# Kernel tuning notes

Hardware: AMD Instinct MI355X
Metric: run time of the kernel (lower is better)

The kernel has to match this reference:

```python
import jax, jax.numpy as jnp
import numpy as np
from jax.scipy.special import logsumexp

EPSILON = 0.1
MAX_ITER = 100
LOG_CLAMP = 1e-30  # matches torch _log_safe clamp(min=1e-30)


def setup_inputs() -> dict:
    key = jax.random.key(0)
    k_c, k_a, k_b = jax.random.split(key, 3)
    B, M, N = 16, 2048, 2048
    C = jax.random.uniform(k_c, (B, M, N), dtype=jnp.float32)  # nonnegative cost matrix
    a = jax.random.uniform(k_a, (B, M), dtype=jnp.float32) + 0.1
    a = a / a.sum(axis=1, keepdims=True)  # source marginal, sums to 1 per batch
    b = jax.random.uniform(k_b, (B, N), dtype=jnp.float32) + 0.1
    b = b / b.sum(axis=1, keepdims=True)  # target marginal
    return {"C": C, "a": a, "b": b}


def reference(C, a, b):
    """Log-domain balanced Sinkhorn (SinkhornDistance.forward, epsilon_scaling=False).

    Returns (distance: (B,), P: (B, M, N)).
    Runs a fixed MAX_ITER iterations (the torch early-break with tol=1e-6 is a
    host-sync convergence shortcut to the same fixed point).
    """
    log_a = jnp.log(jnp.clip(a, LOG_CLAMP))  # (B, M)
    log_b = jnp.log(jnp.clip(b, LOG_CLAMP))  # (B, N)
    log_K = -C / EPSILON  # (B, M, N)
    B, M, N = C.shape
    u0 = jnp.zeros((B, M), dtype=C.dtype)
    v0 = jnp.zeros((B, N), dtype=C.dtype)

    def step(carry, _):
        u, v = carry
        u = log_a - logsumexp(log_K + v[:, None, :], axis=2)  # (B, M)
        v = log_b - logsumexp(log_K + u[:, :, None], axis=1)  # (B, N)
        return (u, v), None

    (u, v), _ = jax.lax.scan(step, (u0, v0), None, length=MAX_ITER)
    log_P = u[:, :, None] + log_K + v[:, None, :]  # (B, M, N)
    P = jnp.exp(log_P)
    distance = jnp.sum(P * C, axis=(1, 2))  # (B,)
    return distance, P
```

## Files before the change

kernel.cpp:

```cpp
#include <hip/hip_runtime.h>
#include <hip/hip_fp16.h>

namespace {

constexpr int NB = 16;
constexpr int MM = 2048;
constexpr int NN = 2048;
constexpr float NEG_INV_EPS = -10.0f;
constexpr int ITERS = 100;


__global__ void __launch_bounds__(256) build_k(const float* __restrict__ C,
                                               __half* __restrict__ K) {
  const size_t stride = (size_t)gridDim.x * blockDim.x * 8;
  const size_t total = (size_t)NB * MM * NN;
  for (size_t i = ((size_t)blockIdx.x * blockDim.x + threadIdx.x) * 8;
       i < total; i += stride) {
    float4 c0 = *reinterpret_cast<const float4*>(C + i);
    float4 c1 = *reinterpret_cast<const float4*>(C + i + 4);
    __half2 h[4];
    h[0] = __floats2half2_rn(__expf(NEG_INV_EPS * c0.x), __expf(NEG_INV_EPS * c0.y));
    h[1] = __floats2half2_rn(__expf(NEG_INV_EPS * c0.z), __expf(NEG_INV_EPS * c0.w));
    h[2] = __floats2half2_rn(__expf(NEG_INV_EPS * c1.x), __expf(NEG_INV_EPS * c1.y));
    h[3] = __floats2half2_rn(__expf(NEG_INV_EPS * c1.z), __expf(NEG_INV_EPS * c1.w));
    *reinterpret_cast<uint4*>(K + i) = *reinterpret_cast<uint4*>(h);
  }
}


__global__ void __launch_bounds__(512, 4) sink_iter_h(
    const __half* __restrict__ Kp,
    const float* __restrict__ a, const float* __restrict__ bm,
    const float* __restrict__ s_cur, float* __restrict__ s_acc,
    float* __restrict__ s_zero, float* __restrict__ z_out) {
  __shared__ __align__(16) __half ksh[2][8][NN];
  __shared__ __align__(16) float wsh[NN];
  __shared__ float zsh[2][8];
  const int b = blockIdx.x >> 5;
  const int chunk = blockIdx.x & 31;
  const int tid = threadIdx.x;
  const int bbase = b * NN;

  {
    const float4 b4 = *reinterpret_cast<const float4*>(bm + bbase + tid * 4);
    const float4 s4 = *reinterpret_cast<const float4*>(s_cur + bbase + tid * 4);
    float4 w4;
    w4.x = b4.x * __builtin_amdgcn_rcpf(s4.x);
    w4.y = b4.y * __builtin_amdgcn_rcpf(s4.y);
    w4.z = b4.z * __builtin_amdgcn_rcpf(s4.z);
    w4.w = b4.w * __builtin_amdgcn_rcpf(s4.w);
    *reinterpret_cast<float4*>(&wsh[tid * 4]) = w4;
  }
  if (tid < 64) s_zero[bbase + chunk * 64 + tid] = 0.0f;
  __syncthreads();

  const int wave = tid >> 6;
  const int lane = tid & 63;

  float wreg[32];
#pragma unroll
  for (int k = 0; k < 4; ++k) {
    const float4* w4 = reinterpret_cast<const float4*>(&wsh[k * 512 + lane * 8]);
    const float4 wa = w4[0], wb = w4[1];
    wreg[k * 8 + 0] = wa.x; wreg[k * 8 + 1] = wa.y;
    wreg[k * 8 + 2] = wa.z; wreg[k * 8 + 3] = wa.w;
    wreg[k * 8 + 4] = wb.x; wreg[k * 8 + 5] = wb.y;
    wreg[k * 8 + 6] = wb.z; wreg[k * 8 + 7] = wb.w;
  }

  const int r0 = chunk * 64;
  const int mycol = tid * 4;
  const size_t abase = (size_t)b * MM;
  float colacc[4] = {0.f, 0.f, 0.f, 0.f};
  uint4 kr[4];

  {
    const int row = r0 + wave;
    const size_t kb = (abase + row) * NN;
    const float av = a[abase + row];
#pragma unroll
    for (int k = 0; k < 4; ++k)
      kr[k] = *reinterpret_cast<const uint4*>(Kp + kb + k * 512 + lane * 8);
    float acc = 0.f;
#pragma unroll
    for (int k = 0; k < 4; ++k) {
      *reinterpret_cast<uint4*>(&ksh[0][wave][k * 512 + lane * 8]) = kr[k];
      const __half2* h = reinterpret_cast<const __half2*>(&kr[k]);
      const float2 f0 = __half22float2(h[0]);
      const float2 f1 = __half22float2(h[1]);
      const float2 f2 = __half22float2(h[2]);
      const float2 f3 = __half22float2(h[3]);
      acc += f0.x * wreg[k * 8 + 0] + f0.y * wreg[k * 8 + 1] +
             f1.x * wreg[k * 8 + 2] + f1.y * wreg[k * 8 + 3] +
             f2.x * wreg[k * 8 + 4] + f2.y * wreg[k * 8 + 5] +
             f3.x * wreg[k * 8 + 6] + f3.y * wreg[k * 8 + 7];
    }
#pragma unroll
    for (int off = 32; off; off >>= 1) acc += __shfl_xor(acc, off, 64);
    const float zv = av * __builtin_amdgcn_rcpf(acc);
    if (lane == 0) {
      zsh[0][wave] = zv;
      z_out[abase + row] = zv;
    }
  }
  __syncthreads();

  for (int sc = 0; sc < 8; ++sc) {
    const int cb = sc & 1, nb = cb ^ 1;
    float av = 0.f;
    if (sc < 7) {
      const int row = r0 + (sc + 1) * 8 + wave;
      const size_t kb = (abase + row) * NN;
      av = a[abase + row];
#pragma unroll
      for (int k = 0; k < 4; ++k)
        kr[k] = *reinterpret_cast<const uint4*>(Kp + kb + k * 512 + lane * 8);
    }
#pragma unroll
    for (int r = 0; r < 8; ++r) {
      const float zi = zsh[cb][r];
      uint2 rv = *reinterpret_cast<const uint2*>(&ksh[cb][r][mycol]);
      const __half2* h = reinterpret_cast<const __half2*>(&rv);
      const float2 f01 = __half22float2(h[0]);
      const float2 f23 = __half22float2(h[1]);
      colacc[0] += f01.x * zi;
      colacc[1] += f01.y * zi;
      colacc[2] += f23.x * zi;
      colacc[3] += f23.y * zi;
    }
    if (sc < 7) {
      const int row = r0 + (sc + 1) * 8 + wave;
      float acc = 0.f;
#pragma unroll
      for (int k = 0; k < 4; ++k) {
        *reinterpret_cast<uint4*>(&ksh[nb][wave][k * 512 + lane * 8]) = kr[k];
        const __half2* h = reinterpret_cast<const __half2*>(&kr[k]);
        const float2 f0 = __half22float2(h[0]);
        const float2 f1 = __half22float2(h[1]);
        const float2 f2 = __half22float2(h[2]);
        const float2 f3 = __half22float2(h[3]);
        acc += f0.x * wreg[k * 8 + 0] + f0.y * wreg[k * 8 + 1] +
               f1.x * wreg[k * 8 + 2] + f1.y * wreg[k * 8 + 3] +
               f2.x * wreg[k * 8 + 4] + f2.y * wreg[k * 8 + 5] +
               f3.x * wreg[k * 8 + 6] + f3.y * wreg[k * 8 + 7];
      }
#pragma unroll
      for (int off = 32; off; off >>= 1) acc += __shfl_xor(acc, off, 64);
      const float zv = av * __builtin_amdgcn_rcpf(acc);
      if (lane == 0) {
        zsh[nb][wave] = zv;
        z_out[abase + row] = zv;
      }
    }
    __syncthreads();
  }

  float* s = s_acc + bbase + mycol;
#pragma unroll
  for (int m = 0; m < 4; ++m) atomicAdd(&s[m], colacc[m]);
}


struct KFromC {
  const float* p;
  __device__ __forceinline__ void load8h(size_t i, float* o, uint4* raw) const {
    float4 c0 = *reinterpret_cast<const float4*>(p + i);
    float4 c1 = *reinterpret_cast<const float4*>(p + i + 4);
    o[0] = __expf(NEG_INV_EPS * c0.x); o[1] = __expf(NEG_INV_EPS * c0.y);
    o[2] = __expf(NEG_INV_EPS * c0.z); o[3] = __expf(NEG_INV_EPS * c0.w);
    o[4] = __expf(NEG_INV_EPS * c1.x); o[5] = __expf(NEG_INV_EPS * c1.y);
    o[6] = __expf(NEG_INV_EPS * c1.z); o[7] = __expf(NEG_INV_EPS * c1.w);
    __half2 h[4];
    h[0] = __floats2half2_rn(o[0], o[1]);
    h[1] = __floats2half2_rn(o[2], o[3]);
    h[2] = __floats2half2_rn(o[4], o[5]);
    h[3] = __floats2half2_rn(o[6], o[7]);
    *raw = *reinterpret_cast<uint4*>(h);
  }
};

template <class KS>
__global__ void __launch_bounds__(512, 4) sink_iter(KS ks,
    const float* __restrict__ a, const float* __restrict__ bm,
    const float* __restrict__ s_cur, float* __restrict__ s_acc,
    float* __restrict__ s_zero, float* __restrict__ z_out) {
  __shared__ __align__(16) __half ksh[16][NN];
  __shared__ __align__(16) float wsh[NN];
  __shared__ float zsh[16];
  const int b = blockIdx.x >> 5;
  const int chunk = blockIdx.x & 31;
  const int tid = threadIdx.x;
  const int bbase = b * NN;

  {
    const float4 b4 = *reinterpret_cast<const float4*>(bm + bbase + tid * 4);
    const float4 s4 = *reinterpret_cast<const float4*>(s_cur + bbase + tid * 4);
    float4 w4;
    w4.x = b4.x * __builtin_amdgcn_rcpf(s4.x);
    w4.y = b4.y * __builtin_amdgcn_rcpf(s4.y);
    w4.z = b4.z * __builtin_amdgcn_rcpf(s4.z);
    w4.w = b4.w * __builtin_amdgcn_rcpf(s4.w);
    *reinterpret_cast<float4*>(&wsh[tid * 4]) = w4;
  }
  if (tid < 64) s_zero[bbase + chunk * 64 + tid] = 0.0f;
  __syncthreads();

  const int wave = tid >> 6;
  const int lane = tid & 63;

  float wreg[32];
#pragma unroll
  for (int k = 0; k < 4; ++k) {
    const float4* w4 = reinterpret_cast<const float4*>(&wsh[k * 512 + lane * 8]);
    const float4 wa = w4[0], wb = w4[1];
    wreg[k * 8 + 0] = wa.x; wreg[k * 8 + 1] = wa.y;
    wreg[k * 8 + 2] = wa.z; wreg[k * 8 + 3] = wa.w;
    wreg[k * 8 + 4] = wb.x; wreg[k * 8 + 5] = wb.y;
    wreg[k * 8 + 6] = wb.z; wreg[k * 8 + 7] = wb.w;
  }

  const int r0 = chunk * 64;
  const int mycol = tid * 4;
  float colacc[4] = {0.f, 0.f, 0.f, 0.f};

  for (int sc = 0; sc < 4; ++sc) {
    const int rowbase = r0 + sc * 16;
#pragma unroll
    for (int rr = 0; rr < 2; ++rr) {
      const int lrow = wave * 2 + rr;
      const int row = rowbase + lrow;
      const size_t kb = ((size_t)(b * MM + row)) * NN;
      float acc = 0.f;
#pragma unroll
      for (int k = 0; k < 4; ++k) {
        float kv[8];
        uint4 raw;
        ks.load8h(kb + k * 512 + lane * 8, kv, &raw);
        *reinterpret_cast<uint4*>(&ksh[lrow][k * 512 + lane * 8]) = raw;
#pragma unroll
        for (int m = 0; m < 8; ++m) acc += kv[m] * wreg[k * 8 + m];
      }
#pragma unroll
      for (int off = 32; off; off >>= 1) acc += __shfl_xor(acc, off, 64);
      if (lane == 0) {
        const float zv = a[b * MM + row] * __builtin_amdgcn_rcpf(acc);
        zsh[lrow] = zv;
        z_out[b * MM + row] = zv;
      }
    }
    __syncthreads();
#pragma unroll 4
    for (int r = 0; r < 16; ++r) {
      const float zi = zsh[r];
      uint2 rv = *reinterpret_cast<const uint2*>(&ksh[r][mycol]);
      const __half2* h = reinterpret_cast<const __half2*>(&rv);
      const float2 f01 = __half22float2(h[0]);
      const float2 f23 = __half22float2(h[1]);
      colacc[0] += f01.x * zi;
      colacc[1] += f01.y * zi;
      colacc[2] += f23.x * zi;
      colacc[3] += f23.y * zi;
    }
    __syncthreads();
  }

  float* s = s_acc + bbase + mycol;
#pragma unroll
  for (int m = 0; m < 4; ++m) atomicAdd(&s[m], colacc[m]);
}


__global__ void __launch_bounds__(256) final_pass(const float* __restrict__ C,
    const float* __restrict__ z, const float* __restrict__ bm,
    const float* __restrict__ s_fin, float* __restrict__ out) {
  __shared__ __align__(16) float wsh[NN];
  __shared__ float zsh[16];
  __shared__ float red[256];
  const int b = blockIdx.x >> 7;
  const int rc = blockIdx.x & 127;
  const int tid = threadIdx.x;
  const int bbase = b * NN;

  for (int j = tid; j < NN; j += 256)
    wsh[j] = bm[bbase + j] * __builtin_amdgcn_rcpf(s_fin[bbase + j]);
  if (tid < 16) zsh[tid] = z[b * MM + rc * 16 + tid];
  __syncthreads();

  float* __restrict__ P = out + NB;
  const int col = tid * 8;
  const float4* w4 = reinterpret_cast<const float4*>(&wsh[col]);
  const float4 wa = w4[0], wb = w4[1];

  float accd = 0.0f;
#pragma unroll 4
  for (int rr = 0; rr < 16; ++rr) {
    const int row = rc * 16 + rr;
    const float zi = zsh[rr];
    const size_t base = ((size_t)(b * MM + row)) * NN + col;
    float4 c0 = *reinterpret_cast<const float4*>(C + base);
    float4 c1 = *reinterpret_cast<const float4*>(C + base + 4);
    float4 p0, p1;
    p0.x = zi * __expf(NEG_INV_EPS * c0.x) * wa.x;
    p0.y = zi * __expf(NEG_INV_EPS * c0.y) * wa.y;
    p0.z = zi * __expf(NEG_INV_EPS * c0.z) * wa.z;
    p0.w = zi * __expf(NEG_INV_EPS * c0.w) * wa.w;
    p1.x = zi * __expf(NEG_INV_EPS * c1.x) * wb.x;
    p1.y = zi * __expf(NEG_INV_EPS * c1.y) * wb.y;
    p1.z = zi * __expf(NEG_INV_EPS * c1.z) * wb.z;
    p1.w = zi * __expf(NEG_INV_EPS * c1.w) * wb.w;
    *reinterpret_cast<float4*>(P + base) = p0;
    *reinterpret_cast<float4*>(P + base + 4) = p1;
    accd += p0.x * c0.x + p0.y * c0.y + p0.z * c0.z + p0.w * c0.w +
            p1.x * c1.x + p1.y * c1.y + p1.z * c1.z + p1.w * c1.w;
  }

  red[tid] = accd;
  __syncthreads();
  if (tid < 128) red[tid] += red[tid + 128];
  __syncthreads();
  if (tid < 64) {
    float v = red[tid] + red[tid + 64];
#pragma unroll
    for (int off = 32; off; off >>= 1) v += __shfl_xor(v, off, 64);
    if (tid == 0) atomicAdd(&out[b], v);
  }
}

}

extern "C" void kernel_launch(void* const* d_in, const int* in_sizes, int n_in,
                              void* d_out, int out_size, void* d_ws, size_t ws_size,
                              hipStream_t stream) {
  const float* C  = (const float*)d_in[0];
  const float* a  = (const float*)d_in[1];
  const float* bm = (const float*)d_in[2];
  float* out = (float*)d_out;
  char* ws = (char*)d_ws;

  const size_t VEC = (size_t)NB * MM * sizeof(float);
  float* z = (float*)(ws);
  float* s[3] = {(float*)(ws + VEC), (float*)(ws + 2 * VEC), (float*)(ws + 3 * VEC)};
  __half* K = (__half*)(ws + 4 * VEC);
  const size_t needK = 4 * VEC + (size_t)NB * MM * NN * sizeof(__half);
  const bool useHalf = (ws_size >= needK);

  hipMemsetAsync(out, 0, NB * sizeof(float), stream);
  hipMemcpyAsync(s[0], bm, (size_t)NB * NN * sizeof(float),
                 hipMemcpyDeviceToDevice, stream);
  hipMemsetAsync(s[1], 0, (size_t)NB * NN * sizeof(float), stream);

  if (useHalf) {
    build_k<<<8192, 256, 0, stream>>>(C, K);
    for (int t = 0; t < ITERS; ++t) {
      sink_iter_h<<<NB * 32, 512, 0, stream>>>(
          K, a, bm, s[t % 3], s[(t + 1) % 3], s[(t + 2) % 3], z);
    }
  } else {
    KFromC ks{C};
    for (int t = 0; t < ITERS; ++t) {
      sink_iter<KFromC><<<NB * 32, 512, 0, stream>>>(
          ks, a, bm, s[t % 3], s[(t + 1) % 3], s[(t + 2) % 3], z);
    }
  }

  final_pass<<<NB * 128, 256, 0, stream>>>(C, z, bm, s[ITERS % 3], out);
}
```

Baseline: 3.594 ms.

## Fuse all Sinkhorn iterations into one cooperative persistent kernel with grid sync

Replaces the 100 separate per-iteration launches with a single cooperative kernel that loops over iterations and uses grid.sync between phases. The column-sum atomics are replaced by per-chunk partial buffers reduced deterministically after a grid barrier, with the scaled weight vector written once for the next iteration. This removes launch overhead and atomic contention but adds two grid-wide barriers per iteration, and it requires all 512 blocks to be co-resident.

```diff
diff --git a/kernel.cpp b/kernel.cpp
--- a/kernel.cpp
+++ b/kernel.cpp
@@ -1,5 +1,8 @@
 #include <hip/hip_runtime.h>
 #include <hip/hip_fp16.h>
+#include <hip/hip_cooperative_groups.h>
+
+namespace cg = cooperative_groups;
 
 namespace {
 
@@ -28,6 +31,155 @@
 }
 
 
+__global__ void __launch_bounds__(512, 4) sink_coop(
+    const __half* __restrict__ Kp,
+    const float* __restrict__ a, const float* __restrict__ bm,
+    float* __restrict__ z_out, float* __restrict__ wbuf,
+    float* __restrict__ partial) {
+  cg::grid_group grid = cg::this_grid();
+  __shared__ __align__(16) __half ksh[2][8][NN];
+  __shared__ __align__(16) float wsh[NN];
+  __shared__ float zsh[2][8];
+  const int b = blockIdx.x >> 5;
+  const int chunk = blockIdx.x & 31;
+  const int tid = threadIdx.x;
+  const int bbase = b * NN;
+  const int wave = tid >> 6;
+  const int lane = tid & 63;
+  const int r0 = chunk * 64;
+  const int mycol = tid * 4;
+  const size_t abase = (size_t)b * MM;
+
+  for (int t = 0; t < ITERS; ++t) {
+    if (t == 0) {
+      *reinterpret_cast<float4*>(&wsh[tid * 4]) = make_float4(1.f, 1.f, 1.f, 1.f);
+    } else {
+      *reinterpret_cast<float4*>(&wsh[tid * 4]) =
+          *reinterpret_cast<const float4*>(wbuf + bbase + tid * 4);
+    }
+    __syncthreads();
+
+    float wreg[32];
+#pragma unroll
+    for (int k = 0; k < 4; ++k) {
+      const float4* w4 = reinterpret_cast<const float4*>(&wsh[k * 512 + lane * 8]);
+      const float4 wa = w4[0], wb = w4[1];
+      wreg[k * 8 + 0] = wa.x; wreg[k * 8 + 1] = wa.y;
+      wreg[k * 8 + 2] = wa.z; wreg[k * 8 + 3] = wa.w;
+      wreg[k * 8 + 4] = wb.x; wreg[k * 8 + 5] = wb.y;
+      wreg[k * 8 + 6] = wb.z; wreg[k * 8 + 7] = wb.w;
+    }
+
+    const bool lastit = (t == ITERS - 1);
+    float colacc[4] = {0.f, 0.f, 0.f, 0.f};
+    uint4 kr[4];
+
+    {
+      const int row = r0 + wave;
+      const size_t kb = (abase + row) * NN;
+      const float av = a[abase + row];
+#pragma unroll
+      for (int k = 0; k < 4; ++k)
+        kr[k] = *reinterpret_cast<const uint4*>(Kp + kb + k * 512 + lane * 8);
+      float acc = 0.f;
+#pragma unroll
+      for (int k = 0; k < 4; ++k) {
+        *reinterpret_cast<uint4*>(&ksh[0][wave][k * 512 + lane * 8]) = kr[k];
+        const __half2* h = reinterpret_cast<const __half2*>(&kr[k]);
+        const float2 f0 = __half22float2(h[0]);
+        const float2 f1 = __half22float2(h[1]);
+        const float2 f2 = __half22float2(h[2]);
+        const float2 f3 = __half22float2(h[3]);
+        acc += f0.x * wreg[k * 8 + 0] + f0.y * wreg[k * 8 + 1] +
+               f1.x * wreg[k * 8 + 2] + f1.y * wreg[k * 8 + 3] +
+               f2.x * wreg[k * 8 + 4] + f2.y * wreg[k * 8 + 5] +
+               f3.x * wreg[k * 8 + 6] + f3.y * wreg[k * 8 + 7];
+      }
+#pragma unroll
+      for (int off = 32; off; off >>= 1) acc += __shfl_xor(acc, off, 64);
+      const float zv = av * __builtin_amdgcn_rcpf(acc);
+      if (lane == 0) {
+        zsh[0][wave] = zv;
+        if (lastit) z_out[abase + row] = zv;
+      }
+    }
+    __syncthreads();
+
+    for (int sc = 0; sc < 8; ++sc) {
+      const int cb = sc & 1, nb2 = cb ^ 1;
+      float av = 0.f;
+      if (sc < 7) {
+        const int row = r0 + (sc + 1) * 8 + wave;
+        const size_t kb = (abase + row) * NN;
+        av = a[abase + row];
+#pragma unroll
+        for (int k = 0; k < 4; ++k)
+          kr[k] = *reinterpret_cast<const uint4*>(Kp + kb + k * 512 + lane * 8);
+      }
+#pragma unroll
+      for (int r = 0; r < 8; ++r) {
+        const float zi = zsh[cb][r];
+        uint2 rv = *reinterpret_cast<const uint2*>(&ksh[cb][r][mycol]);
+        const __half2* h = reinterpret_cast<const __half2*>(&rv);
+        const float2 f01 = __half22float2(h[0]);
+        const float2 f23 = __half22float2(h[1]);
+        colacc[0] += f01.x * zi;
+        colacc[1] += f01.y * zi;
+        colacc[2] += f23.x * zi;
+        colacc[3] += f23.y * zi;
+      }
+      if (sc < 7) {
+        const int row = r0 + (sc + 1) * 8 + wave;
+        float acc = 0.f;
+#pragma unroll
+        for (int k = 0; k < 4; ++k) {
+          *reinterpret_cast<uint4*>(&ksh[nb2][wave][k * 512 + lane * 8]) = kr[k];
+          const __half2* h = reinterpret_cast<const __half2*>(&kr[k]);
+          const float2 f0 = __half22float2(h[0]);
+          const float2 f1 = __half22float2(h[1]);
+          const float2 f2 = __half22float2(h[2]);
+          const float2 f3 = __half22float2(h[3]);
+          acc += f0.x * wreg[k * 8 + 0] + f0.y * wreg[k * 8 + 1] +
+                 f1.x * wreg[k * 8 + 2] + f1.y * wreg[k * 8 + 3] +
+                 f2.x * wreg[k * 8 + 4] + f2.y * wreg[k * 8 + 5] +
+                 f3.x * wreg[k * 8 + 6] + f3.y * wreg[k * 8 + 7];
+        }
+#pragma unroll
+        for (int off = 32; off; off >>= 1) acc += __shfl_xor(acc, off, 64);
+        const float zv = av * __builtin_amdgcn_rcpf(acc);
+        if (lane == 0) {
+          zsh[nb2][wave] = zv;
+          if (lastit) z_out[abase + row] = zv;
+        }
+      }
+      __syncthreads();
+    }
+
+    *reinterpret_cast<float4*>(partial + ((size_t)(b * 32 + chunk)) * NN + mycol) =
+        make_float4(colacc[0], colacc[1], colacc[2], colacc[3]);
+    __threadfence();
+    grid.sync();
+
+    if (tid < 64) {
+      const int col = chunk * 64 + tid;
+      const float* pp = partial + (size_t)b * 32 * NN + col;
+      float s0 = 0.f, s1 = 0.f, s2 = 0.f, s3 = 0.f;
+#pragma unroll
+      for (int c = 0; c < 32; c += 4) {
+        s0 += pp[(size_t)(c + 0) * NN];
+        s1 += pp[(size_t)(c + 1) * NN];
+        s2 += pp[(size_t)(c + 2) * NN];
+        s3 += pp[(size_t)(c + 3) * NN];
+      }
+      const float sv = (s0 + s1) + (s2 + s3);
+      wbuf[bbase + col] = bm[bbase + col] * __builtin_amdgcn_rcpf(sv);
+    }
+    __threadfence();
+    grid.sync();
+  }
+}
+
+
 __global__ void __launch_bounds__(512, 4) sink_iter_h(
     const __half* __restrict__ Kp,
     const float* __restrict__ a, const float* __restrict__ bm,
@@ -106,7 +258,7 @@
   __syncthreads();
 
   for (int sc = 0; sc < 8; ++sc) {
-    const int cb = sc & 1, nb = cb ^ 1;
+    const int cb = sc & 1, nb2 = cb ^ 1;
     float av = 0.f;
     if (sc < 7) {
       const int row = r0 + (sc + 1) * 8 + wave;
@@ -133,7 +285,7 @@
       float acc = 0.f;
 #pragma unroll
       for (int k = 0; k < 4; ++k) {
-        *reinterpret_cast<uint4*>(&ksh[nb][wave][k * 512 + lane * 8]) = kr[k];
+        *reinterpret_cast<uint4*>(&ksh[nb2][wave][k * 512 + lane * 8]) = kr[k];
         const __half2* h = reinterpret_cast<const __half2*>(&kr[k]);
         const float2 f0 = __half22float2(h[0]);
         const float2 f1 = __half22float2(h[1]);
@@ -148,7 +300,7 @@
       for (int off = 32; off; off >>= 1) acc += __shfl_xor(acc, off, 64);
       const float zv = av * __builtin_amdgcn_rcpf(acc);
       if (lane == 0) {
-        zsh[nb][wave] = zv;
+        zsh[nb2][wave] = zv;
         z_out[abase + row] = zv;
       }
     }
@@ -272,7 +424,7 @@
 
 __global__ void __launch_bounds__(256) final_pass(const float* __restrict__ C,
     const float* __restrict__ z, const float* __restrict__ bm,
-    const float* __restrict__ s_fin, float* __restrict__ out) {
+    const float* __restrict__ sw, const int is_w, float* __restrict__ out) {
   __shared__ __align__(16) float wsh[NN];
   __shared__ float zsh[16];
   __shared__ float red[256];
@@ -282,7 +434,8 @@
   const int bbase = b * NN;
 
   for (int j = tid; j < NN; j += 256)
-    wsh[j] = bm[bbase + j] * __builtin_amdgcn_rcpf(s_fin[bbase + j]);
+    wsh[j] = is_w ? sw[bbase + j]
+                  : bm[bbase + j] * __builtin_amdgcn_rcpf(sw[bbase + j]);
   if (tid < 16) zsh[tid] = z[b * MM + rc * 16 + tid];
   __syncthreads();
 
@@ -338,13 +491,34 @@
   char* ws = (char*)d_ws;
 
   const size_t VEC = (size_t)NB * MM * sizeof(float);
+  const size_t PART = (size_t)NB * 32 * NN * sizeof(float);
+  const size_t KBYTES = (size_t)NB * MM * NN * sizeof(__half);
+
+  hipMemsetAsync(out, 0, NB * sizeof(float), stream);
+
+  int maxb = 0;
+  (void)hipOccupancyMaxActiveBlocksPerMultiprocessor(&maxb, sink_coop, 512, 0);
+  const bool canCoop = (maxb >= 2) && (ws_size >= 2 * VEC + PART + KBYTES);
+
+  if (canCoop) {
+    float* z = (float*)(ws);
+    float* wbuf = (float*)(ws + VEC);
+    float* partial = (float*)(ws + 2 * VEC);
+    __half* K = (__half*)(ws + 2 * VEC + PART);
+    build_k<<<8192, 256, 0, stream>>>(C, K);
+    void* args[6] = {(void*)&K, (void*)&a, (void*)&bm,
+                     (void*)&z, (void*)&wbuf, (void*)&partial};
+    hipLaunchCooperativeKernel((const void*)sink_coop, dim3(NB * 32), dim3(512),
+                               args, 0, stream);
+    final_pass<<<NB * 128, 256, 0, stream>>>(C, z, bm, wbuf, 1, out);
+    return;
+  }
+
   float* z = (float*)(ws);
   float* s[3] = {(float*)(ws + VEC), (float*)(ws + 2 * VEC), (float*)(ws + 3 * VEC)};
   __half* K = (__half*)(ws + 4 * VEC);
-  const size_t needK = 4 * VEC + (size_t)NB * MM * NN * sizeof(__half);
-  const bool useHalf = (ws_size >= needK);
-
-  hipMemsetAsync(out, 0, NB * sizeof(float), stream);
+  const bool useHalf = (ws_size >= 4 * VEC + KBYTES);
+
   hipMemcpyAsync(s[0], bm, (size_t)NB * NN * sizeof(float),
                  hipMemcpyDeviceToDevice, stream);
   hipMemsetAsync(s[1], 0, (size_t)NB * NN * sizeof(float), stream);
@@ -363,5 +537,5 @@
     }
   }
 
-  final_pass<<<NB * 128, 256, 0, stream>>>(C, z, bm, s[ITERS % 3], out);
-}
+  final_pass<<<NB * 128, 256, 0, stream>>>(C, z, bm, s[ITERS % 3], 0, out);
+}
```

After: 3.546 ms. Within noise of the previous version (-1.4%).
